# Kernel optimization log

Measured on AMD Instinct MI355X. Metric: run time of the kernel, lower is better.

The kernel has to match this reference:

```python
import jax, jax.numpy as jnp
import numpy as np

OBJ_D, LANG_D, GEO_D, HID = 320, 256, 6, 256
PAIR_D = 2 * OBJ_D + GEO_D + LANG_D  # 902


def _l2norm(x, eps=1e-12):
    n = jnp.linalg.norm(x, axis=-1, keepdims=True)
    return x / jnp.maximum(n, eps)


def setup_inputs() -> dict:
    key = jax.random.key(0)
    ks = jax.random.split(key, 8)
    B, N = 2, 512
    object_embeddings = jax.random.normal(ks[0], (B, N, OBJ_D), dtype=jnp.float32)
    object_geometry = jax.random.normal(ks[1], (B, N, GEO_D), dtype=jnp.float32)
    utterance_features = jax.random.normal(ks[2], (B, LANG_D), dtype=jnp.float32)
    # MLP params (xavier-ish with gain 0.1, zero bias, as in the torch init)
    lim1 = 0.1 * np.sqrt(6.0 / (PAIR_D + HID))
    W1 = jax.random.uniform(ks[3], (PAIR_D, HID), minval=-lim1, maxval=lim1, dtype=jnp.float32)
    b1 = jnp.zeros((HID,), jnp.float32)
    lim2 = 0.1 * np.sqrt(6.0 / (HID + 1))
    W2 = jax.random.uniform(ks[4], (HID,), minval=-lim2, maxval=lim2, dtype=jnp.float32)
    b2 = jnp.zeros((), jnp.float32)
    return {"object_embeddings": object_embeddings, "object_geometry": object_geometry,
            "utterance_features": utterance_features, "W1": W1, "b1": b1, "W2": W2, "b2": b2}


def reference(object_embeddings, object_geometry, utterance_features, W1, b1, W2, b2):
    # L2-normalize embeddings and language (F.normalize, eps=1e-12)
    emb = _l2norm(object_embeddings)          # [B,N,D]
    lang = _l2norm(utterance_features)        # [B,L]
    geom = object_geometry                    # [B,N,G]

    # The torch module concatenates [obj_i, obj_j, geom_j - geom_i, lang] -> Linear.
    # Decompose the first Linear by input slices: mathematically identical,
    # avoids materializing the [B,N,N,902] concat tensor.
    Wi = W1[:OBJ_D]                            # [D,H]
    Wj = W1[OBJ_D:2 * OBJ_D]                   # [D,H]
    Wg = W1[2 * OBJ_D:2 * OBJ_D + GEO_D]       # [G,H]
    Wl = W1[2 * OBJ_D + GEO_D:]                # [L,H]

    hi = jnp.einsum('bnd,dh->bnh', emb, Wi) - jnp.einsum('bng,gh->bnh', geom, Wg)  # i terms
    hj = jnp.einsum('bnd,dh->bnh', emb, Wj) + jnp.einsum('bng,gh->bnh', geom, Wg)  # j terms
    hl = jnp.einsum('bl,lh->bh', lang, Wl) + b1                                     # lang + bias

    # hidden: [B,N,N,H]; exact (erf) GELU to match torch nn.GELU default
    h = jax.nn.gelu(hi[:, :, None, :] + hj[:, None, :, :] + hl[:, None, None, :],
                    approximate=False)
    scores = jnp.einsum('bijh,h->bij', h, W2) + b2  # [B,N,N] all_pair_scores

    # temperature == 1.0; no candidate_mask -> plain stable softmax over j
    pair_weights = jax.nn.softmax(scores, axis=-1)                    # [B,N,N]
    relation_context = jnp.einsum('bij,bjd->bid', pair_weights, emb)  # [B,N,D]
    relation_scores = jnp.sum(pair_weights * scores, axis=-1)         # 'weighted' aggregation
    return relation_scores, relation_context
```

## Files before the change

kernel.cpp:

```cpp
#include <hip/hip_runtime.h>
#include <hip/hip_fp16.h>
#include <math.h>

#define OBJ_D 320
#define LANG_D 256
#define GEO_D 6
#define HID 256
#define NN 512
#define BATCH 2

#define GK0 0.3989422804014327f
#define GK1 (-0.066490380066905448f)

__device__ __forceinline__ float wave_allreduce_sum(float v) {
#pragma unroll
    for (int o = 32; o > 0; o >>= 1) v += __shfl_xor(v, o, 64);
    return v;
}
__device__ __forceinline__ float wave_allreduce_max(float v) {
#pragma unroll
    for (int o = 32; o > 0; o >>= 1) v = fmaxf(v, __shfl_xor(v, o, 64));
    return v;
}

__global__ __launch_bounds__(512) void k_pre(const float* __restrict__ emb,
                                             const float* __restrict__ geom,
                                             const float* __restrict__ utter,
                                             const float* __restrict__ W1,
                                             const float* __restrict__ b1,
                                             const float* __restrict__ W2,
                                             float* __restrict__ emb_n,
                                             float* __restrict__ hi_p,
                                             __half2* __restrict__ hj2T,
                                             float* __restrict__ hl,
                                             float* __restrict__ Dj,
                                             float* __restrict__ Cip,
                                             float* __restrict__ Chl) {
    int tid = threadIdx.x;
    int w = tid >> 6, lane = tid & 63;
    int half = tid >> 8, h = tid & 255;

    __shared__ float4 esT4[OBJ_D];
    __shared__ float gs[4][GEO_D];
    __shared__ float rn[4];
    __shared__ float pAI[2][4][HID];
    __shared__ float pAJ[2][4][HID];
    __shared__ float red[8];
    __shared__ float redD[4][4], redC[4][4];
    float* esT = (float*)esT4;

    if (blockIdx.x >= 256) {
        int b = blockIdx.x - 256;
        float* lcomb = esT;
        float v = (half == 0) ? utter[b * LANG_D + h] : 0.0f;
        float ss = wave_allreduce_sum(v * v);
        if (lane == 0) red[w] = ss;
        __syncthreads();
        if (tid == 0) {
            float t = red[0] + red[1] + red[2] + red[3] +
                      red[4] + red[5] + red[6] + red[7];
            red[0] = 1.0f / fmaxf(sqrtf(t), 1e-12f);
        }
        __syncthreads();
        float* lang_s = esT + 512;
        if (half == 0) lang_s[h] = v * red[0];
        __syncthreads();
        const float* Wl = W1 + (size_t)(2 * OBJ_D + GEO_D) * HID + h;
        float acc = (half == 0) ? b1[h] : 0.0f;
#pragma unroll 8
        for (int l = half * 128; l < half * 128 + 128; l++)
            acc = fmaf(lang_s[l], Wl[(size_t)l * HID], acc);
        lcomb[half * 256 + h] = acc;
        __syncthreads();
        if (half == 0) {
            float a = lcomb[h] + lcomb[256 + h];
            hl[b * HID + h] = a;
            float cpart = wave_allreduce_sum(W2[h] * a);
            if (lane == 0) red[w] = cpart;
        }
        __syncthreads();
        if (tid == 0) Chl[b] = red[0] + red[1] + red[2] + red[3];
        return;
    }

    const int R = 4;
    int b = blockIdx.x & 1;
    int n0 = (blockIdx.x >> 1) * R;
    int dbase = 160 * half;

    const float* WiC = W1 + h;
    const float* WjC = W1 + (size_t)OBJ_D * HID + h;
    float wi[16], wj[16], win[16], wjn[16];
#pragma unroll
    for (int k = 0; k < 16; k++) {
        wi[k] = WiC[(size_t)(dbase + k) * HID];
        wj[k] = WjC[(size_t)(dbase + k) * HID];
    }

    const float* esrc = emb + (size_t)(b * NN + n0) * OBJ_D;
    float ev[3]; int eidx[3]; int ecnt = 0;
    for (int idx = tid; idx < R * OBJ_D; idx += 512) {
        float x = esrc[idx];
        ev[ecnt] = x; eidx[ecnt] = idx; ecnt++;
        esT[(idx % OBJ_D) * 4 + (idx / OBJ_D)] = x;
    }
    if (tid < R * GEO_D) gs[tid / GEO_D][tid % GEO_D] = geom[(size_t)(b * NN + n0) * GEO_D + tid];
    __syncthreads();
    if (w < 4) {
        float s = 0.0f;
#pragma unroll
        for (int k = lane; k < OBJ_D; k += 64) { float x = esT[k * 4 + w]; s += x * x; }
        s = wave_allreduce_sum(s);
        if (lane == 0) rn[w] = 1.0f / fmaxf(sqrtf(s), 1e-12f);
    }
    __syncthreads();
    float* edst = emb_n + (size_t)(b * NN + n0) * OBJ_D;
    for (int c = 0; c < ecnt; c++) {
        int idx = eidx[c];
        float nv = ev[c] * rn[idx / OBJ_D];
        esT[(idx % OBJ_D) * 4 + (idx / OBJ_D)] = nv;
        edst[idx] = nv;
    }
    __syncthreads();

    float ai[R] = {0, 0, 0, 0}, aj[R] = {0, 0, 0, 0};
    for (int g = 0; g < 160; g += 16) {
        if (g + 16 < 160) {
#pragma unroll
            for (int k = 0; k < 16; k++) {
                win[k] = WiC[(size_t)(dbase + g + 16 + k) * HID];
                wjn[k] = WjC[(size_t)(dbase + g + 16 + k) * HID];
            }
        }
#pragma unroll
        for (int k = 0; k < 16; k++) {
            float4 e4 = esT4[dbase + g + k];
            ai[0] = fmaf(e4.x, wi[k], ai[0]); aj[0] = fmaf(e4.x, wj[k], aj[0]);
            ai[1] = fmaf(e4.y, wi[k], ai[1]); aj[1] = fmaf(e4.y, wj[k], aj[1]);
            ai[2] = fmaf(e4.z, wi[k], ai[2]); aj[2] = fmaf(e4.z, wj[k], aj[2]);
            ai[3] = fmaf(e4.w, wi[k], ai[3]); aj[3] = fmaf(e4.w, wj[k], aj[3]);
        }
#pragma unroll
        for (int k = 0; k < 16; k++) { wi[k] = win[k]; wj[k] = wjn[k]; }
    }
#pragma unroll
    for (int r = 0; r < R; r++) { pAI[half][r][h] = ai[r]; pAJ[half][r][h] = aj[r]; }
    __syncthreads();

    if (half == 0) {
        float gw[GEO_D];
#pragma unroll
        for (int g = 0; g < GEO_D; g++) gw[g] = W1[(size_t)(2 * OBJ_D + g) * HID + h];
        float w2v = W2[h];
        float yi[R], vj[R];
#pragma unroll
        for (int r = 0; r < R; r++) {
            float A = pAI[0][r][h] + pAI[1][r][h];
            float J = pAJ[0][r][h] + pAJ[1][r][h];
            float gp = 0.0f;
#pragma unroll
            for (int g = 0; g < GEO_D; g++) gp = fmaf(gs[r][g], gw[g], gp);
            yi[r] = A - gp;
            vj[r] = J + gp;
            hi_p[(size_t)(b * NN + n0 + r) * HID + h] = yi[r];
        }
        {
            __half2 p0 = __floats2half2_rn(vj[0], vj[1]);
            __half2 p1 = __floats2half2_rn(vj[2], vj[3]);
            __half2* dst = hj2T + ((size_t)(b * 256 + h) * 256 + (n0 >> 1));
            dst[0] = p0;
            dst[1] = p1;
        }
#pragma unroll
        for (int r = 0; r < R; r++) {
            float ds = wave_allreduce_sum(w2v * vj[r]);
            float cs = wave_allreduce_sum(w2v * yi[r]);
            if (lane == 0) { redD[w][r] = ds; redC[w][r] = cs; }
        }
    }
    __syncthreads();
    if (tid < R) {
        Dj[b * NN + n0 + tid]  = redD[0][tid] + redD[1][tid] + redD[2][tid] + redD[3][tid];
        Cip[b * NN + n0 + tid] = redC[0][tid] + redC[1][tid] + redC[2][tid] + redC[3][tid];
    }
}

union H2U { uint2 u; __half2 h[2]; };

__global__ __launch_bounds__(1024) void k_main(const float* __restrict__ hi_p,
                                               const __half2* __restrict__ hj2T,
                                               const float* __restrict__ emb_n,
                                               const float* __restrict__ hl,
                                               const float* __restrict__ W2,
                                               const float* __restrict__ b2p,
                                               const float* __restrict__ Dj,
                                               const float* __restrict__ Cip,
                                               const float* __restrict__ Chl,
                                               float* __restrict__ out) {
    int b = blockIdx.x & 1;
    int i0 = (blockIdx.x >> 1) * 4;
    int tid = threadIdx.x;
    int w = tid >> 6, lane = tid & 63;
    int s = w >> 1;
    int rg = w & 1;

    __shared__ __half2 xw2[4][HID];
    __shared__ __half2 w2d[HID];
    __shared__ __half2 scp[8][4][256];
    __shared__ float4 pq4[NN];
    __shared__ float part[16][4 * OBJ_D + 4];
    __shared__ float redx[4][4], redsum[4][4], reddot[4][4];

    const uint2* hjq = (const uint2*)(hj2T + (size_t)b * 256 * 256) + (64 * rg + lane);
    int h0 = s * 32;
    H2U v[8], vn[8];
#pragma unroll
    for (int k = 0; k < 8; k++) v[k].u = hjq[(size_t)(h0 + k) * 128];

    for (int idx = tid; idx < 5 * HID; idx += 1024) {
        int r = idx >> 8, h = idx & 255;
        if (r < 4) {
            float x = hi_p[(size_t)(b * NN + i0 + r) * HID + h] + hl[b * HID + h];
            xw2[r][h] = __floats2half2_rn(x, x);
        } else {
            float wsc = W2[h] * 64.0f;
            w2d[h] = __floats2half2_rn(wsc, wsc);
        }
    }
    __syncthreads();

    const __half2 K0h = __floats2half2_rn(GK0, GK0);
    const __half2 K1h = __floats2half2_rn(GK1, GK1);
    __half2 acc2[4][2];
#pragma unroll
    for (int r = 0; r < 4; r++)
#pragma unroll
        for (int q = 0; q < 2; q++) acc2[r][q] = __floats2half2_rn(0.0f, 0.0f);

    for (int g = 0; g < 4; g++) {
        if (g + 1 < 4) {
#pragma unroll
            for (int k = 0; k < 8; k++) vn[k].u = hjq[(size_t)(h0 + (g + 1) * 8 + k) * 128];
        }
#pragma unroll
        for (int k = 0; k < 8; k++) {
            int h = h0 + g * 8 + k;
            __half2 x0 = xw2[0][h], x1 = xw2[1][h], x2 = xw2[2][h], x3 = xw2[3][h];
            __half2 ww = w2d[h];
#pragma unroll
            for (int q = 0; q < 2; q++) {
                __half2 vv = v[k].h[q];
                __half2 a0 = __hadd2(vv, x0), a1 = __hadd2(vv, x1);
                __half2 a2 = __hadd2(vv, x2), a3 = __hadd2(vv, x3);
                __half2 t0 = __hmul2(a0, a0), t1 = __hmul2(a1, a1);
                __half2 t2 = __hmul2(a2, a2), t3 = __hmul2(a3, a3);
                __half2 q0 = __hfma2(t0, K1h, K0h), q1 = __hfma2(t1, K1h, K0h);
                __half2 q2 = __hfma2(t2, K1h, K0h), q3 = __hfma2(t3, K1h, K0h);
                __half2 m0 = __hmul2(t0, q0), m1 = __hmul2(t1, q1);
                __half2 m2 = __hmul2(t2, q2), m3 = __hmul2(t3, q3);
                acc2[0][q] = __hfma2(m0, ww, acc2[0][q]);
                acc2[1][q] = __hfma2(m1, ww, acc2[1][q]);
                acc2[2][q] = __hfma2(m2, ww, acc2[2][q]);
                acc2[3][q] = __hfma2(m3, ww, acc2[3][q]);
            }
        }
#pragma unroll
        for (int k = 0; k < 8; k++) v[k] = vn[k];
    }
    {
        int jp0 = 128 * rg + 2 * lane;
#pragma unroll
        for (int r = 0; r < 4; r++) {
            H2U o; o.h[0] = acc2[r][0]; o.h[1] = acc2[r][1];
            *(uint2*)&scp[s][r][jp0] = o.u;
        }
    }

    float Ci[4];
#pragma unroll
    for (int r = 0; r < 4; r++) Ci[r] = Cip[b * NN + i0 + r] + Chl[b];
    __syncthreads();

    const float inv64 = 1.0f / 64.0f;
    float cs[4][2];
    if (tid < 256) {
        int jp = tid;
        float2 dj2 = ((const float2*)Dj)[b * 256 + jp];
#pragma unroll
        for (int r = 0; r < 4; r++) {
            float lo = 0.0f, hi = 0.0f;
#pragma unroll
            for (int s8 = 0; s8 < 8; s8++) {
                float2 f = __half22float2(scp[s8][r][jp]);
                lo += f.x; hi += f.y;
            }
            cs[r][0] = lo * inv64 + 0.5f * (Ci[r] + dj2.x);
            cs[r][1] = hi * inv64 + 0.5f * (Ci[r] + dj2.y);
        }
#pragma unroll
        for (int r = 0; r < 4; r++) {
            float m = wave_allreduce_max(fmaxf(cs[r][0], cs[r][1]));
            if (lane == 0) redx[w][r] = m;
        }
    }
    __syncthreads();
    float M[4];
#pragma unroll
    for (int r = 0; r < 4; r++)
        M[r] = fmaxf(fmaxf(redx[0][r], redx[1][r]), fmaxf(redx[2][r], redx[3][r]));
    float ex[4][2];
    if (tid < 256) {
#pragma unroll
        for (int r = 0; r < 4; r++) {
            ex[r][0] = expf(cs[r][0] - M[r]);
            ex[r][1] = expf(cs[r][1] - M[r]);
            float qs = wave_allreduce_sum(ex[r][0] + ex[r][1]);
            float qd = wave_allreduce_sum(ex[r][0] * cs[r][0] + ex[r][1] * cs[r][1]);
            if (lane == 0) { redsum[w][r] = qs; reddot[w][r] = qd; }
        }
    }
    __syncthreads();
    float inv[4];
#pragma unroll
    for (int r = 0; r < 4; r++) {
        float S = redsum[0][r] + redsum[1][r] + redsum[2][r] + redsum[3][r];
        inv[r] = 1.0f / S;
    }
    if (tid < 256) {
        int p = tid;
        float4 pa, pb;
        pa.x = ex[0][0] * inv[0]; pa.y = ex[1][0] * inv[1];
        pa.z = ex[2][0] * inv[2]; pa.w = ex[3][0] * inv[3];
        pb.x = ex[0][1] * inv[0]; pb.y = ex[1][1] * inv[1];
        pb.z = ex[2][1] * inv[2]; pb.w = ex[3][1] * inv[3];
        pq4[2 * p] = pa;
        pq4[2 * p + 1] = pb;
    }
    if (tid == 0) {
        float b2 = b2p[0];
#pragma unroll
        for (int r = 0; r < 4; r++) {
            float D = reddot[0][r] + reddot[1][r] + reddot[2][r] + reddot[3][r];
            out[b * NN + i0 + r] = D * inv[r] + b2;
        }
    }
    __syncthreads();

    const float* eb = emb_n + (size_t)b * NN * OBJ_D;
    float ac[4][5];
#pragma unroll
    for (int r = 0; r < 4; r++)
#pragma unroll
        for (int c = 0; c < 5; c++) ac[r][c] = 0.0f;
    int jbase = w * 32;
#pragma unroll 4
    for (int jj = 0; jj < 32; jj++) {
        float4 qq = pq4[jbase + jj];
        const float* e = eb + (size_t)(jbase + jj) * OBJ_D + lane;
#pragma unroll
        for (int c = 0; c < 5; c++) {
            float evv = e[64 * c];
            ac[0][c] = fmaf(qq.x, evv, ac[0][c]);
            ac[1][c] = fmaf(qq.y, evv, ac[1][c]);
            ac[2][c] = fmaf(qq.z, evv, ac[2][c]);
            ac[3][c] = fmaf(qq.w, evv, ac[3][c]);
        }
    }
#pragma unroll
    for (int r = 0; r < 4; r++)
#pragma unroll
        for (int c = 0; c < 5; c++) part[w][r * OBJ_D + c * 64 + lane] = ac[r][c];
    __syncthreads();

    for (int item = tid; item < 4 * OBJ_D; item += 1024) {
        float ssum = 0.0f;
#pragma unroll
        for (int ww2 = 0; ww2 < 16; ww2++) ssum += part[ww2][item];
        int r = item / OBJ_D, d = item - r * OBJ_D;
        out[BATCH * NN + (size_t)(b * NN + i0 + r) * OBJ_D + d] = ssum;
    }
}

extern "C" void kernel_launch(void* const* d_in, const int* in_sizes, int n_in,
                              void* d_out, int out_size, void* d_ws, size_t ws_size,
                              hipStream_t stream) {
    const float* emb   = (const float*)d_in[0];
    const float* geom  = (const float*)d_in[1];
    const float* utter = (const float*)d_in[2];
    const float* W1    = (const float*)d_in[3];
    const float* b1    = (const float*)d_in[4];
    const float* W2    = (const float*)d_in[5];
    const float* b2    = (const float*)d_in[6];
    float* out = (float*)d_out;

    float* ws = (float*)d_ws;
    float* hl    = ws;
    float* emb_n = ws + 512;
    float* hi_p  = emb_n + BATCH * NN * OBJ_D;
    float* hj2f  = hi_p + BATCH * NN * HID;
    float* Dj    = hj2f + BATCH * 256 * 256;
    float* Cip   = Dj + BATCH * NN;
    float* Chl   = Cip + BATCH * NN;
    __half2* hj2T = (__half2*)hj2f;

    hipLaunchKernelGGL(k_pre, dim3(256 + BATCH), dim3(512), 0, stream,
                       emb, geom, utter, W1, b1, W2, emb_n, hi_p, hj2T, hl, Dj, Cip, Chl);
    hipLaunchKernelGGL(k_main, dim3(BATCH * NN / 4), dim3(1024), 0, stream,
                       hi_p, hj2T, emb_n, hl, W2, b2, Dj, Cip, Chl, out);
}
```

Baseline: 111.8 us.

## Fuse pre and main kernels into one cooperative kernel with grid sync

Merges the precompute kernel and the pairwise-score kernel into a single cooperative launch of 256 blocks of 1024 threads, separated by a grid-wide barrier. Each block now computes its own rows' hi and the language projection locally in shared memory, so the hi_p/hl/Cip/Chl round-trips through global memory disappear. Only hj and Dj are still exchanged across blocks. This removes one launch and the inter-kernel gap but adds a grid sync. Every block also recomputes the language GEMV redundantly, and the precompute phase moves to 1024-thread blocks with a 4-way split.

```diff
diff --git a/kernel.cpp b/kernel.cpp
--- a/kernel.cpp
+++ b/kernel.cpp
@@ -1,6 +1,9 @@
 #include <hip/hip_runtime.h>
 #include <hip/hip_fp16.h>
+#include <hip/hip_cooperative_groups.h>
 #include <math.h>
+
+namespace cg = cooperative_groups;
 
 #define OBJ_D 320
 #define LANG_D 256
@@ -23,97 +26,76 @@
     return v;
 }
 
-__global__ __launch_bounds__(512) void k_pre(const float* __restrict__ emb,
-                                             const float* __restrict__ geom,
-                                             const float* __restrict__ utter,
-                                             const float* __restrict__ W1,
-                                             const float* __restrict__ b1,
-                                             const float* __restrict__ W2,
-                                             float* __restrict__ emb_n,
-                                             float* __restrict__ hi_p,
-                                             __half2* __restrict__ hj2T,
-                                             float* __restrict__ hl,
-                                             float* __restrict__ Dj,
-                                             float* __restrict__ Cip,
-                                             float* __restrict__ Chl) {
+union H2U { uint2 u; __half2 h[2]; };
+
+__global__ __launch_bounds__(1024) void k_fused(const float* __restrict__ emb,
+                                                const float* __restrict__ geom,
+                                                const float* __restrict__ utter,
+                                                const float* __restrict__ W1,
+                                                const float* __restrict__ b1,
+                                                const float* __restrict__ W2,
+                                                const float* __restrict__ b2p,
+                                                float* __restrict__ emb_n,
+                                                __half2* __restrict__ hj2T,
+                                                float* __restrict__ Dj,
+                                                float* __restrict__ out) {
     int tid = threadIdx.x;
     int w = tid >> 6, lane = tid & 63;
-    int half = tid >> 8, h = tid & 255;
-
-    __shared__ float4 esT4[OBJ_D];
-    __shared__ float gs[4][GEO_D];
-    __shared__ float rn[4];
-    __shared__ float pAI[2][4][HID];
-    __shared__ float pAJ[2][4][HID];
-    __shared__ float red[8];
-    __shared__ float redD[4][4], redC[4][4];
-    float* esT = (float*)esT4;
-
-    if (blockIdx.x >= 256) {
-        int b = blockIdx.x - 256;
-        float* lcomb = esT;
-        float v = (half == 0) ? utter[b * LANG_D + h] : 0.0f;
-        float ss = wave_allreduce_sum(v * v);
-        if (lane == 0) red[w] = ss;
-        __syncthreads();
-        if (tid == 0) {
-            float t = red[0] + red[1] + red[2] + red[3] +
-                      red[4] + red[5] + red[6] + red[7];
-            red[0] = 1.0f / fmaxf(sqrtf(t), 1e-12f);
-        }
-        __syncthreads();
-        float* lang_s = esT + 512;
-        if (half == 0) lang_s[h] = v * red[0];
-        __syncthreads();
-        const float* Wl = W1 + (size_t)(2 * OBJ_D + GEO_D) * HID + h;
-        float acc = (half == 0) ? b1[h] : 0.0f;
-#pragma unroll 8
-        for (int l = half * 128; l < half * 128 + 128; l++)
-            acc = fmaf(lang_s[l], Wl[(size_t)l * HID], acc);
-        lcomb[half * 256 + h] = acc;
-        __syncthreads();
-        if (half == 0) {
-            float a = lcomb[h] + lcomb[256 + h];
-            hl[b * HID + h] = a;
-            float cpart = wave_allreduce_sum(W2[h] * a);
-            if (lane == 0) red[w] = cpart;
-        }
-        __syncthreads();
-        if (tid == 0) Chl[b] = red[0] + red[1] + red[2] + red[3];
-        return;
-    }
-
-    const int R = 4;
-    int b = blockIdx.x & 1;
-    int n0 = (blockIdx.x >> 1) * R;
-    int dbase = 160 * half;
+    int qd = tid >> 8, h = tid & 255;
+    int blk = blockIdx.x;
+    int b = blk & 1;
+    int n0 = (blk >> 1) * 4;
+
+    __shared__ __half2 xw2[4][HID];
+    __shared__ __half2 w2d[HID];
+    __shared__ __half2 scp[8][4][256];
+    __shared__ float4 pq4[NN];
+    __shared__ alignas(16) float part[16][4 * OBJ_D + 4];
+    __shared__ float gs[4][GEO_D], rn[4];
+    __shared__ float red[16], redD[4][4], redC[4][4], CiS[4];
+
+    float* pool = &part[0][0];
+    float4* esT4 = (float4*)pool;
+    float* esT = pool;
+    float* pAI = pool + 1280;
+    float* pAJ = pool + 5376;
+    float* langN = pool + 9472;
+    float* lcomb = langN + 256;
 
     const float* WiC = W1 + h;
     const float* WjC = W1 + (size_t)OBJ_D * HID + h;
-    float wi[16], wj[16], win[16], wjn[16];
-#pragma unroll
-    for (int k = 0; k < 16; k++) {
+    int dbase = 80 * qd;
+    float wi[8], wj[8], win[8], wjn[8];
+#pragma unroll
+    for (int k = 0; k < 8; k++) {
         wi[k] = WiC[(size_t)(dbase + k) * HID];
         wj[k] = WjC[(size_t)(dbase + k) * HID];
     }
 
     const float* esrc = emb + (size_t)(b * NN + n0) * OBJ_D;
-    float ev[3]; int eidx[3]; int ecnt = 0;
-    for (int idx = tid; idx < R * OBJ_D; idx += 512) {
+    float ev[2]; int eidx[2]; int ecnt = 0;
+    for (int idx = tid; idx < 4 * OBJ_D; idx += 1024) {
         float x = esrc[idx];
         ev[ecnt] = x; eidx[ecnt] = idx; ecnt++;
         esT[(idx % OBJ_D) * 4 + (idx / OBJ_D)] = x;
     }
-    if (tid < R * GEO_D) gs[tid / GEO_D][tid % GEO_D] = geom[(size_t)(b * NN + n0) * GEO_D + tid];
-    __syncthreads();
+    if (tid < 4 * GEO_D) gs[tid / GEO_D][tid % GEO_D] = geom[(size_t)(b * NN + n0) * GEO_D + tid];
+    if (tid < 256) { float wsc = W2[tid] * 64.0f; w2d[tid] = __floats2half2_rn(wsc, wsc); }
+    float uv = (tid < 256) ? utter[b * LANG_D + tid] : 0.0f;
+    __syncthreads();
+
     if (w < 4) {
         float s = 0.0f;
 #pragma unroll
         for (int k = lane; k < OBJ_D; k += 64) { float x = esT[k * 4 + w]; s += x * x; }
         s = wave_allreduce_sum(s);
         if (lane == 0) rn[w] = 1.0f / fmaxf(sqrtf(s), 1e-12f);
-    }
-    __syncthreads();
+        float ls = wave_allreduce_sum(uv * uv);
+        if (lane == 0) red[8 + w] = ls;
+    }
+    __syncthreads();
+    if (tid == 0)
+        red[15] = 1.0f / fmaxf(sqrtf(red[8] + red[9] + red[10] + red[11]), 1e-12f);
     float* edst = emb_n + (size_t)(b * NN + n0) * OBJ_D;
     for (int c = 0; c < ecnt; c++) {
         int idx = eidx[c];
@@ -122,47 +104,65 @@
         edst[idx] = nv;
     }
     __syncthreads();
-
-    float ai[R] = {0, 0, 0, 0}, aj[R] = {0, 0, 0, 0};
-    for (int g = 0; g < 160; g += 16) {
-        if (g + 16 < 160) {
-#pragma unroll
-            for (int k = 0; k < 16; k++) {
-                win[k] = WiC[(size_t)(dbase + g + 16 + k) * HID];
-                wjn[k] = WjC[(size_t)(dbase + g + 16 + k) * HID];
+    if (tid < 256) langN[tid] = uv * red[15];
+
+    float ai[4] = {0, 0, 0, 0}, aj4[4] = {0, 0, 0, 0};
+    for (int g = 0; g < 80; g += 8) {
+        if (g + 8 < 80) {
+#pragma unroll
+            for (int k = 0; k < 8; k++) {
+                win[k] = WiC[(size_t)(dbase + g + 8 + k) * HID];
+                wjn[k] = WjC[(size_t)(dbase + g + 8 + k) * HID];
             }
         }
 #pragma unroll
-        for (int k = 0; k < 16; k++) {
+        for (int k = 0; k < 8; k++) {
             float4 e4 = esT4[dbase + g + k];
-            ai[0] = fmaf(e4.x, wi[k], ai[0]); aj[0] = fmaf(e4.x, wj[k], aj[0]);
-            ai[1] = fmaf(e4.y, wi[k], ai[1]); aj[1] = fmaf(e4.y, wj[k], aj[1]);
-            ai[2] = fmaf(e4.z, wi[k], ai[2]); aj[2] = fmaf(e4.z, wj[k], aj[2]);
-            ai[3] = fmaf(e4.w, wi[k], ai[3]); aj[3] = fmaf(e4.w, wj[k], aj[3]);
-        }
-#pragma unroll
-        for (int k = 0; k < 16; k++) { wi[k] = win[k]; wj[k] = wjn[k]; }
-    }
-#pragma unroll
-    for (int r = 0; r < R; r++) { pAI[half][r][h] = ai[r]; pAJ[half][r][h] = aj[r]; }
-    __syncthreads();
-
-    if (half == 0) {
+            ai[0] = fmaf(e4.x, wi[k], ai[0]); aj4[0] = fmaf(e4.x, wj[k], aj4[0]);
+            ai[1] = fmaf(e4.y, wi[k], ai[1]); aj4[1] = fmaf(e4.y, wj[k], aj4[1]);
+            ai[2] = fmaf(e4.z, wi[k], ai[2]); aj4[2] = fmaf(e4.z, wj[k], aj4[2]);
+            ai[3] = fmaf(e4.w, wi[k], ai[3]); aj4[3] = fmaf(e4.w, wj[k], aj4[3]);
+        }
+#pragma unroll
+        for (int k = 0; k < 8; k++) { wi[k] = win[k]; wj[k] = wjn[k]; }
+    }
+#pragma unroll
+    for (int r = 0; r < 4; r++) {
+        pAI[qd * 1024 + r * 256 + h] = ai[r];
+        pAJ[qd * 1024 + r * 256 + h] = aj4[r];
+    }
+    __syncthreads();
+
+    {
+        const float* Wl = W1 + (size_t)(2 * OBJ_D + GEO_D) * HID + h;
+        float acc = 0.0f;
+#pragma unroll 8
+        for (int l = qd * 64; l < qd * 64 + 64; l++)
+            acc = fmaf(langN[l], Wl[(size_t)l * HID], acc);
+        lcomb[qd * 256 + h] = acc;
+    }
+    __syncthreads();
+
+    if (qd == 0) {
+        float hlval = b1[h] + lcomb[h] + lcomb[256 + h] + lcomb[512 + h] + lcomb[768 + h];
         float gw[GEO_D];
 #pragma unroll
         for (int g = 0; g < GEO_D; g++) gw[g] = W1[(size_t)(2 * OBJ_D + g) * HID + h];
         float w2v = W2[h];
-        float yi[R], vj[R];
-#pragma unroll
-        for (int r = 0; r < R; r++) {
-            float A = pAI[0][r][h] + pAI[1][r][h];
-            float J = pAJ[0][r][h] + pAJ[1][r][h];
+        float yi[4], vj[4];
+#pragma unroll
+        for (int r = 0; r < 4; r++) {
+            float A = pAI[r * 256 + h] + pAI[1024 + r * 256 + h] +
+                      pAI[2048 + r * 256 + h] + pAI[3072 + r * 256 + h];
+            float J = pAJ[r * 256 + h] + pAJ[1024 + r * 256 + h] +
+                      pAJ[2048 + r * 256 + h] + pAJ[3072 + r * 256 + h];
             float gp = 0.0f;
 #pragma unroll
             for (int g = 0; g < GEO_D; g++) gp = fmaf(gs[r][g], gw[g], gp);
             yi[r] = A - gp;
             vj[r] = J + gp;
-            hi_p[(size_t)(b * NN + n0 + r) * HID + h] = yi[r];
+            float x = yi[r] + hlval;
+            xw2[r][h] = __floats2half2_rn(x, x);
         }
         {
             __half2 p0 = __floats2half2_rn(vj[0], vj[1]);
@@ -172,63 +172,32 @@
             dst[1] = p1;
         }
 #pragma unroll
-        for (int r = 0; r < R; r++) {
+        for (int r = 0; r < 4; r++) {
             float ds = wave_allreduce_sum(w2v * vj[r]);
             float cs = wave_allreduce_sum(w2v * yi[r]);
             if (lane == 0) { redD[w][r] = ds; redC[w][r] = cs; }
         }
-    }
-    __syncthreads();
-    if (tid < R) {
-        Dj[b * NN + n0 + tid]  = redD[0][tid] + redD[1][tid] + redD[2][tid] + redD[3][tid];
-        Cip[b * NN + n0 + tid] = redC[0][tid] + redC[1][tid] + redC[2][tid] + redC[3][tid];
-    }
-}
-
-union H2U { uint2 u; __half2 h[2]; };
-
-__global__ __launch_bounds__(1024) void k_main(const float* __restrict__ hi_p,
-                                               const __half2* __restrict__ hj2T,
-                                               const float* __restrict__ emb_n,
-                                               const float* __restrict__ hl,
-                                               const float* __restrict__ W2,
-                                               const float* __restrict__ b2p,
-                                               const float* __restrict__ Dj,
-                                               const float* __restrict__ Cip,
-                                               const float* __restrict__ Chl,
-                                               float* __restrict__ out) {
-    int b = blockIdx.x & 1;
-    int i0 = (blockIdx.x >> 1) * 4;
-    int tid = threadIdx.x;
-    int w = tid >> 6, lane = tid & 63;
+        float cl = wave_allreduce_sum(w2v * hlval);
+        if (lane == 0) red[w] = cl;
+    }
+    __syncthreads();
+    if (tid < 4) {
+        Dj[b * NN + n0 + tid] = redD[0][tid] + redD[1][tid] + redD[2][tid] + redD[3][tid];
+        float Chl = (red[0] + red[1] + red[2] + red[3]) * 0.25f;
+        Chl = red[0] + red[1] + red[2] + red[3];
+        CiS[tid] = redC[0][tid] + redC[1][tid] + redC[2][tid] + redC[3][tid] + Chl;
+    }
+    __threadfence();
+    cg::this_grid().sync();
+
     int s = w >> 1;
     int rg = w & 1;
-
-    __shared__ __half2 xw2[4][HID];
-    __shared__ __half2 w2d[HID];
-    __shared__ __half2 scp[8][4][256];
-    __shared__ float4 pq4[NN];
-    __shared__ float part[16][4 * OBJ_D + 4];
-    __shared__ float redx[4][4], redsum[4][4], reddot[4][4];
-
     const uint2* hjq = (const uint2*)(hj2T + (size_t)b * 256 * 256) + (64 * rg + lane);
     int h0 = s * 32;
     H2U v[8], vn[8];
 #pragma unroll
     for (int k = 0; k < 8; k++) v[k].u = hjq[(size_t)(h0 + k) * 128];
 
-    for (int idx = tid; idx < 5 * HID; idx += 1024) {
-        int r = idx >> 8, h = idx & 255;
-        if (r < 4) {
-            float x = hi_p[(size_t)(b * NN + i0 + r) * HID + h] + hl[b * HID + h];
-            xw2[r][h] = __floats2half2_rn(x, x);
-        } else {
-            float wsc = W2[h] * 64.0f;
-            w2d[h] = __floats2half2_rn(wsc, wsc);
-        }
-    }
-    __syncthreads();
-
     const __half2 K0h = __floats2half2_rn(GK0, GK0);
     const __half2 K1h = __floats2half2_rn(GK1, GK1);
     __half2 acc2[4][2];
@@ -244,9 +213,9 @@
         }
 #pragma unroll
         for (int k = 0; k < 8; k++) {
-            int h = h0 + g * 8 + k;
-            __half2 x0 = xw2[0][h], x1 = xw2[1][h], x2 = xw2[2][h], x3 = xw2[3][h];
-            __half2 ww = w2d[h];
+            int hh = h0 + g * 8 + k;
+            __half2 x0 = xw2[0][hh], x1 = xw2[1][hh], x2 = xw2[2][hh], x3 = xw2[3][hh];
+            __half2 ww = w2d[hh];
 #pragma unroll
             for (int q = 0; q < 2; q++) {
                 __half2 vv = v[k].h[q];
@@ -275,14 +244,13 @@
             *(uint2*)&scp[s][r][jp0] = o.u;
         }
     }
-
     float Ci[4];
 #pragma unroll
-    for (int r = 0; r < 4; r++) Ci[r] = Cip[b * NN + i0 + r] + Chl[b];
+    for (int r = 0; r < 4; r++) Ci[r] = CiS[r];
     __syncthreads();
 
     const float inv64 = 1.0f / 64.0f;
-    float cs[4][2];
+    float cs2[4][2];
     if (tid < 256) {
         int jp = tid;
         float2 dj2 = ((const float2*)Dj)[b * 256 + jp];
@@ -294,36 +262,36 @@
                 float2 f = __half22float2(scp[s8][r][jp]);
                 lo += f.x; hi += f.y;
             }
-            cs[r][0] = lo * inv64 + 0.5f * (Ci[r] + dj2.x);
-            cs[r][1] = hi * inv64 + 0.5f * (Ci[r] + dj2.y);
-        }
-#pragma unroll
-        for (int r = 0; r < 4; r++) {
-            float m = wave_allreduce_max(fmaxf(cs[r][0], cs[r][1]));
-            if (lane == 0) redx[w][r] = m;
+            cs2[r][0] = lo * inv64 + 0.5f * (Ci[r] + dj2.x);
+            cs2[r][1] = hi * inv64 + 0.5f * (Ci[r] + dj2.y);
+        }
+#pragma unroll
+        for (int r = 0; r < 4; r++) {
+            float m = wave_allreduce_max(fmaxf(cs2[r][0], cs2[r][1]));
+            if (lane == 0) redD[w][r] = m;
         }
     }
     __syncthreads();
     float M[4];
 #pragma unroll
     for (int r = 0; r < 4; r++)
-        M[r] = fmaxf(fmaxf(redx[0][r], redx[1][r]), fmaxf(redx[2][r], redx[3][r]));
+        M[r] = fmaxf(fmaxf(redD[0][r], redD[1][r]), fmaxf(redD[2][r], redD[3][r]));
     float ex[4][2];
     if (tid < 256) {
 #pragma unroll
         for (int r = 0; r < 4; r++) {
-            ex[r][0] = expf(cs[r][0] - M[r]);
-            ex[r][1] = expf(cs[r][1] - M[r]);
+            ex[r][0] = expf(cs2[r][0] - M[r]);
+            ex[r][1] = expf(cs2[r][1] - M[r]);
             float qs = wave_allreduce_sum(ex[r][0] + ex[r][1]);
-            float qd = wave_allreduce_sum(ex[r][0] * cs[r][0] + ex[r][1] * cs[r][1]);
-            if (lane == 0) { redsum[w][r] = qs; reddot[w][r] = qd; }
+            float qd2 = wave_allreduce_sum(ex[r][0] * cs2[r][0] + ex[r][1] * cs2[r][1]);
+            if (lane == 0) { redC[w][r] = qs; red[4 * w + r] = qd2; }
         }
     }
     __syncthreads();
     float inv[4];
 #pragma unroll
     for (int r = 0; r < 4; r++) {
-        float S = redsum[0][r] + redsum[1][r] + redsum[2][r] + redsum[3][r];
+        float S = redC[0][r] + redC[1][r] + redC[2][r] + redC[3][r];
         inv[r] = 1.0f / S;
     }
     if (tid < 256) {
@@ -340,8 +308,8 @@
         float b2 = b2p[0];
 #pragma unroll
         for (int r = 0; r < 4; r++) {
-            float D = reddot[0][r] + reddot[1][r] + reddot[2][r] + reddot[3][r];
-            out[b * NN + i0 + r] = D * inv[r] + b2;
+            float D = red[r] + red[4 + r] + red[8 + r] + red[12 + r];
+            out[b * NN + n0 + r] = D * inv[r] + b2;
         }
     }
     __syncthreads();
@@ -377,7 +345,7 @@
 #pragma unroll
         for (int ww2 = 0; ww2 < 16; ww2++) ssum += part[ww2][item];
         int r = item / OBJ_D, d = item - r * OBJ_D;
-        out[BATCH * NN + (size_t)(b * NN + i0 + r) * OBJ_D + d] = ssum;
+        out[BATCH * NN + (size_t)(b * NN + n0 + r) * OBJ_D + d] = ssum;
     }
 }
 
@@ -394,17 +362,14 @@
     float* out = (float*)d_out;
 
     float* ws = (float*)d_ws;
-    float* hl    = ws;
-    float* emb_n = ws + 512;
-    float* hi_p  = emb_n + BATCH * NN * OBJ_D;
-    float* hj2f  = hi_p + BATCH * NN * HID;
-    float* Dj    = hj2f + BATCH * 256 * 256;
-    float* Cip   = Dj + BATCH * NN;
-    float* Chl   = Cip + BATCH * NN;
+    float* emb_n = ws;
+    float* hj2f  = emb_n + BATCH * NN * OBJ_D;
+    float* Djp   = hj2f + BATCH * 256 * 256;
     __half2* hj2T = (__half2*)hj2f;
 
-    hipLaunchKernelGGL(k_pre, dim3(256 + BATCH), dim3(512), 0, stream,
-                       emb, geom, utter, W1, b1, W2, emb_n, hi_p, hj2T, hl, Dj, Cip, Chl);
-    hipLaunchKernelGGL(k_main, dim3(BATCH * NN / 4), dim3(1024), 0, stream,
-                       hi_p, hj2T, emb_n, hl, W2, b2, Dj, Cip, Chl, out);
+    void* args[] = {(void*)&emb, (void*)&geom, (void*)&utter, (void*)&W1,
+                    (void*)&b1, (void*)&W2, (void*)&b2,
+                    (void*)&emb_n, (void*)&hj2T, (void*)&Djp, (void*)&out};
+    hipLaunchCooperativeKernel((const void*)k_fused, dim3(256), dim3(1024),
+                               args, 0, stream);
 }
```

Result: slower. 196.8 us (+75.9%).
